# Performance work log

Measured on AMD Instinct MI355X. Metric: run time of the kernel, lower is better.

## Reference

```python
import jax, jax.numpy as jnp
import numpy as np

SEQ, BATCH, IN_DIM, HID, OUT = 512, 256, 300, 256, 2


def setup_inputs() -> dict:
    key = jax.random.key(0)
    ks = jax.random.split(key, 7)
    s_ih = 1.0 / np.sqrt(HID)
    return {
        "x": jax.random.normal(ks[0], (SEQ, BATCH, IN_DIM), jnp.float32),
        "W_ih": jax.random.uniform(ks[1], (HID, IN_DIM), jnp.float32, -s_ih, s_ih),
        "W_hh": jax.random.uniform(ks[2], (HID, HID), jnp.float32, -s_ih, s_ih),
        "b_ih": jax.random.uniform(ks[3], (HID,), jnp.float32, -s_ih, s_ih),
        "b_hh": jax.random.uniform(ks[4], (HID,), jnp.float32, -s_ih, s_ih),
        "W_fc": jax.random.uniform(ks[5], (OUT, HID), jnp.float32, -s_ih, s_ih),
        "b_fc": jax.random.uniform(ks[6], (OUT,), jnp.float32, -s_ih, s_ih),
    }


def reference(x, W_ih, W_hh, b_ih, b_hh, W_fc, b_fc):
    # Precompute input projection for all timesteps at once: [T, B, H]
    xp = jnp.einsum('tbi,hi->tbh', x, W_ih) + b_ih + b_hh

    def step(h, xt):
        h_new = jnp.tanh(xt + h @ W_hh.T)
        return h_new, None

    h0 = jnp.zeros((x.shape[1], W_hh.shape[0]), x.dtype)
    hT, _ = jax.lax.scan(step, h0, xp)  # hT: [B, H]
    # Dropout(0.3) is identity in eval mode.
    logits = hT @ W_fc.T + b_fc  # [B, 2]
    return jax.nn.log_softmax(logits, axis=-1)
```

## Files before the change

kernel.cpp:

```cpp
#include <hip/hip_runtime.h>
#include <hip/hip_bf16.h>
#include <cstdint>
#include <cstddef>

#define SEQ 512
#define BATCH 256
#define IN_DIM 300
#define HID 256

typedef __attribute__((ext_vector_type(8))) short bf16x8;
typedef __attribute__((ext_vector_type(4))) float f32x4;
typedef __attribute__((ext_vector_type(4))) unsigned int u32x4;

__device__ __forceinline__ unsigned short f2bf(float f) {
  union { float f; unsigned int u; } v; v.f = f;
  unsigned int u = v.u;
  return (unsigned short)((u + 0x7fffu + ((u >> 16) & 1u)) >> 16);
}
__device__ __forceinline__ unsigned short f2bf_fast(float f) {
  union { float f; unsigned int u; } v; v.f = f;
  return (unsigned short)((v.u + 0x8000u) >> 16);
}
__device__ __forceinline__ float bitsf(unsigned int u) {
  union { unsigned int u; float f; } v; v.u = u; return v.f;
}
__device__ __forceinline__ unsigned int cvtpk(float lo, float hi) {
  union { __hip_bfloat162 h; unsigned int u; } c;
  c.h = __float22bfloat162_rn(make_float2(lo, hi));
  return c.u;
}
__device__ __forceinline__ bf16x8 cvt8(float a0,float a1,float a2,float a3,
                                       float a4,float a5,float a6,float a7) {
  union { __hip_bfloat162 h2[4]; bf16x8 v; } c;
  c.h2[0] = __float22bfloat162_rn(make_float2(a0, a1));
  c.h2[1] = __float22bfloat162_rn(make_float2(a2, a3));
  c.h2[2] = __float22bfloat162_rn(make_float2(a4, a5));
  c.h2[3] = __float22bfloat162_rn(make_float2(a6, a7));
  return c.v;
}
__device__ __forceinline__ void barrier_lgkm() {
  asm volatile("s_waitcnt lgkmcnt(0)" ::: "memory");
  __builtin_amdgcn_s_barrier();
  asm volatile("" ::: "memory");
}

__global__ __launch_bounds__(256) void conv_wih(const float* __restrict__ w,
                                                unsigned short* __restrict__ w_bf) {
  int idx = blockIdx.x * 256 + threadIdx.x;
  int n = idx / 320, k = idx - n * 320;
  float v = (k < IN_DIM) ? w[n * IN_DIM + k] : 0.f;
  w_bf[idx] = f2bf(v);
}

__global__ __launch_bounds__(512) void gemm_xp(const float* __restrict__ x,
    const unsigned short* __restrict__ w_bf, const float* __restrict__ b_ih,
    const float* __restrict__ b_hh, unsigned int* __restrict__ xp2)
{
  __shared__ unsigned int a_lds[128][20];
  const int tid  = threadIdx.x;
  const int wave = tid >> 6;
  const int lane = tid & 63;
  const int l15  = lane & 15;
  const int quad = lane >> 4;
  const long m0  = (long)blockIdx.x * 128;

  bf16x8 wf[2][10];
  #pragma unroll
  for (int nt = 0; nt < 2; ++nt) {
    const unsigned short* wp = w_bf + (size_t)(wave*32 + nt*16 + l15) * 320 + quad*8;
    #pragma unroll
    for (int kc = 0; kc < 10; ++kc)
      wf[nt][kc] = *(const bf16x8*)(wp + kc*32);
  }

  f32x4 acc[8][2];
  #pragma unroll
  for (int mt = 0; mt < 8; ++mt) {
    acc[mt][0] = (f32x4){0.f, 0.f, 0.f, 0.f};
    acc[mt][1] = (f32x4){0.f, 0.f, 0.f, 0.f};
  }

  const int ar = tid >> 2;
  const int ac = (tid & 3) * 8;
  const float* xrow = x + (size_t)(m0 + ar) * IN_DIM;

  float av[8];
  {
    float2 p0 = *(const float2*)(xrow + ac + 0);
    float2 p1 = *(const float2*)(xrow + ac + 2);
    float2 p2 = *(const float2*)(xrow + ac + 4);
    float2 p3 = *(const float2*)(xrow + ac + 6);
    av[0]=p0.x; av[1]=p0.y; av[2]=p1.x; av[3]=p1.y;
    av[4]=p2.x; av[5]=p2.y; av[6]=p3.x; av[7]=p3.y;
  }

  #pragma unroll
  for (int kc = 0; kc < 10; ++kc) {
    u32x4 pk;
    pk.x = cvtpk(av[0], av[1]);
    pk.y = cvtpk(av[2], av[3]);
    pk.z = cvtpk(av[4], av[5]);
    pk.w = cvtpk(av[6], av[7]);
    *(u32x4*)&a_lds[ar][(tid & 3) * 4] = pk;
    barrier_lgkm();
    if (kc < 9) {
      const int k0 = (kc + 1) * 32;
      const float* src = xrow + k0 + ac;
      if (k0 + ac + 8 <= IN_DIM) {
        float2 p0 = *(const float2*)(src + 0);
        float2 p1 = *(const float2*)(src + 2);
        float2 p2 = *(const float2*)(src + 4);
        float2 p3 = *(const float2*)(src + 6);
        av[0]=p0.x; av[1]=p0.y; av[2]=p1.x; av[3]=p1.y;
        av[4]=p2.x; av[5]=p2.y; av[6]=p3.x; av[7]=p3.y;
      } else {
        #pragma unroll
        for (int j = 0; j < 8; ++j) av[j] = (k0 + ac + j < IN_DIM) ? src[j] : 0.f;
      }
    }
    #pragma unroll
    for (int mt = 0; mt < 8; ++mt) {
      bf16x8 afr = *(const bf16x8*)&a_lds[mt*16 + l15][quad*4];
      acc[mt][0] = __builtin_amdgcn_mfma_f32_16x16x32_bf16(afr, wf[0][kc], acc[mt][0], 0, 0, 0);
      acc[mt][1] = __builtin_amdgcn_mfma_f32_16x16x32_bf16(afr, wf[1][kc], acc[mt][1], 0, 0, 0);
    }
    barrier_lgkm();
  }

  const int t  = (int)(blockIdx.x >> 1);
  const int b4 = ((int)blockIdx.x & 1) * 32;
  #pragma unroll
  for (int nt = 0; nt < 2; ++nt) {
    const int n = wave*32 + nt*16 + l15;
    const float kb = 2.0f * (b_ih[n] + b_hh[n]);
    const int tid_lo = wave*64 + nt*16 + l15;
    #pragma unroll
    for (int mt = 0; mt < 8; ++mt) {
      const int g = b4 + mt*4 + quad;
      const size_t base = ((size_t)t*64 + g) * 512;
      float y0 = fmaf(2.0f, acc[mt][nt][0], kb);
      float y1 = fmaf(2.0f, acc[mt][nt][1], kb);
      float y2 = fmaf(2.0f, acc[mt][nt][2], kb);
      float y3 = fmaf(2.0f, acc[mt][nt][3], kb);
      xp2[base + tid_lo]      = cvtpk(y0, y1);
      xp2[base + tid_lo + 32] = cvtpk(y2, y3);
    }
  }
}

__global__ __launch_bounds__(512) void rnn_scan(const float* __restrict__ W_hh,
    const unsigned int* __restrict__ xp2, float* __restrict__ hT)
{
  __shared__ alignas(16) unsigned short hbuf[2][4 * 272];
  const int tid  = threadIdx.x;
  const int wave = tid >> 6;
  const int lane = tid & 63;
  const int l15  = lane & 15;
  const int quad = lane >> 4;
  const int g = blockIdx.x;
  const int c0 = wave * 32;

  bf16x8 wf[2][8];
  #pragma unroll
  for (int nt = 0; nt < 2; ++nt) {
    const int n = c0 + nt*16 + l15;
    #pragma unroll
    for (int kc = 0; kc < 8; ++kc) {
      const float* src = W_hh + n*HID + kc*32 + quad*8;
      float4 p0 = *(const float4*)src;
      float4 p1 = *(const float4*)(src + 4);
      wf[nt][kc] = cvt8(p0.x,p0.y,p0.z,p0.w,p1.x,p1.y,p1.z,p1.w);
    }
  }

  const int rb    = (quad >> 1) * 2;
  const int col_e = c0 + (quad & 1) * 16 + l15;
  const int abase = (l15 & 3) * 272 + quad * 8;

  for (int i = tid; i < 4 * 272; i += 512) hbuf[0][i] = 0;

  const unsigned int* xbase = xp2 + (size_t)g * 512 + tid;

  __syncthreads();

  unsigned int xq[16], xqn[16];
  #pragma unroll
  for (int j = 0; j < 16; ++j)
    xq[j] = xbase[(size_t)j * 32768];

  for (int tc = 0; tc < SEQ / 16; ++tc) {
    if (tc < SEQ/16 - 1) {
      const unsigned int* pn = xbase + (size_t)(tc + 1) * 16 * 32768;
      #pragma unroll
      for (int j = 0; j < 16; ++j)
        xqn[j] = pn[(size_t)j * 32768];
    }
    #pragma unroll
    for (int j = 0; j < 16; ++j) {
      const int cur = j & 1;
      bf16x8 afr[8];
      #pragma unroll
      for (int kc = 0; kc < 8; ++kc)
        afr[kc] = *(const bf16x8*)&hbuf[cur][abase + kc*32];
      f32x4 a0A = (f32x4){0.f,0.f,0.f,0.f}, a0B = a0A, a1A = a0A, a1B = a0A;
      #pragma unroll
      for (int kc = 0; kc < 8; kc += 2) {
        a0A = __builtin_amdgcn_mfma_f32_16x16x32_bf16(afr[kc],   wf[0][kc],   a0A, 0, 0, 0);
        a1A = __builtin_amdgcn_mfma_f32_16x16x32_bf16(afr[kc],   wf[1][kc],   a1A, 0, 0, 0);
        a0B = __builtin_amdgcn_mfma_f32_16x16x32_bf16(afr[kc+1], wf[0][kc+1], a0B, 0, 0, 0);
        a1B = __builtin_amdgcn_mfma_f32_16x16x32_bf16(afr[kc+1], wf[1][kc+1], a1B, 0, 0, 0);
      }
      f32x4 acc0 = a0A + a0B;
      f32x4 acc1 = a1A + a1B;
      f32x4 a = (quad & 1) ? acc1 : acc0;
      float s0 = (quad >> 1) ? a[2] : a[0];
      float s1 = (quad >> 1) ? a[3] : a[1];
      float xv0 = bitsf(xq[j] << 16);
      float xv1 = bitsf(xq[j] & 0xffff0000u);
      float y0 = fmaf(2.0f, s0, xv0);
      float y1 = fmaf(2.0f, s1, xv1);
      float h0 = fmaf(-2.0f, __builtin_amdgcn_rcpf(__expf(y0) + 1.0f), 1.0f);
      float h1 = fmaf(-2.0f, __builtin_amdgcn_rcpf(__expf(y1) + 1.0f), 1.0f);
      if (j < 15 || tc < SEQ/16 - 1) {
        hbuf[1 - cur][ rb      * 272 + col_e] = f2bf_fast(h0);
        hbuf[1 - cur][(rb + 1) * 272 + col_e] = f2bf_fast(h1);
      } else {
        hT[(size_t)(g*4 + rb    ) * HID + col_e] = h0;
        hT[(size_t)(g*4 + rb + 1) * HID + col_e] = h1;
      }
      barrier_lgkm();
    }
    if (tc < SEQ/16 - 1) {
      #pragma unroll
      for (int j = 0; j < 16; ++j)
        xq[j] = xqn[j];
    }
  }
}

__global__ __launch_bounds__(64) void fc_head(const float* __restrict__ hT,
    const float* __restrict__ W_fc, const float* __restrict__ b_fc,
    float* __restrict__ out)
{
  const int b = blockIdx.x;
  const int l = threadIdx.x;
  float s0 = 0.f, s1 = 0.f;
  #pragma unroll
  for (int j0 = 0; j0 < HID; j0 += 64) {
    float h = hT[(size_t)b * HID + j0 + l];
    s0 += h * W_fc[j0 + l];
    s1 += h * W_fc[HID + j0 + l];
  }
  #pragma unroll
  for (int off = 32; off > 0; off >>= 1) {
    s0 += __shfl_xor(s0, off, 64);
    s1 += __shfl_xor(s1, off, 64);
  }
  if (l == 0) {
    float l0 = s0 + b_fc[0], l1 = s1 + b_fc[1];
    float m = fmaxf(l0, l1);
    float lse = m + logf(expf(l0 - m) + expf(l1 - m));
    out[b*2 + 0] = l0 - lse;
    out[b*2 + 1] = l1 - lse;
  }
}

extern "C" void kernel_launch(void* const* d_in, const int* in_sizes, int n_in,
                              void* d_out, int out_size, void* d_ws, size_t ws_size,
                              hipStream_t stream) {
  const float* x    = (const float*)d_in[0];
  const float* W_ih = (const float*)d_in[1];
  const float* W_hh = (const float*)d_in[2];
  const float* b_ih = (const float*)d_in[3];
  const float* b_hh = (const float*)d_in[4];
  const float* W_fc = (const float*)d_in[5];
  const float* b_fc = (const float*)d_in[6];
  float* out = (float*)d_out;

  const size_t xp_bytes = (size_t)SEQ * BATCH * HID * 2;
  const size_t wb_bytes = (size_t)256 * 320 * 2;
  const size_t ht_bytes = (size_t)BATCH * HID * 4;
  if (ws_size < xp_bytes + wb_bytes + ht_bytes) return;

  char* ws = (char*)d_ws;
  unsigned int*   xp2  = (unsigned int*)ws;
  unsigned short* w_bf = (unsigned short*)(ws + xp_bytes);
  float*          hT   = (float*)(ws + xp_bytes + wb_bytes);

  hipLaunchKernelGGL(conv_wih, dim3(320),  dim3(256), 0, stream, W_ih, w_bf);
  hipLaunchKernelGGL(gemm_xp,  dim3(1024), dim3(512), 0, stream, x, w_bf, b_ih, b_hh, xp2);
  hipLaunchKernelGGL(rnn_scan, dim3(64),   dim3(512), 0, stream, W_hh, xp2, hT);
  hipLaunchKernelGGL(fc_head,  dim3(BATCH), dim3(64), 0, stream, hT, W_fc, b_fc, out);
}
```

Baseline: 492.5 us.

## Fuse input projection and FC head into the recurrent scan kernel

Each recurrent block now computes its own input projection on the fly, one window of 8 timesteps at a time. It stages x in LDS as bf16 and runs a small MFMA GEMM between windows, which removes the large xp intermediate written to and read from global memory and the separate gemm_xp launch. The next window's x rows are prefetched into registers during the scan steps. The FC head and log-softmax also move into the same kernel via LDS, which drops the hT round trip and a launch. In exchange, the input GEMM now runs on only 64 blocks and sits on the serial critical path between windows, so it can lengthen the scan.

```diff
diff --git a/kernel.cpp b/kernel.cpp
--- a/kernel.cpp
+++ b/kernel.cpp
@@ -10,7 +10,6 @@
 
 typedef __attribute__((ext_vector_type(8))) short bf16x8;
 typedef __attribute__((ext_vector_type(4))) float f32x4;
-typedef __attribute__((ext_vector_type(4))) unsigned int u32x4;
 
 __device__ __forceinline__ unsigned short f2bf(float f) {
   union { float f; unsigned int u; } v; v.f = f;
@@ -47,120 +46,86 @@
 __global__ __launch_bounds__(256) void conv_wih(const float* __restrict__ w,
                                                 unsigned short* __restrict__ w_bf) {
   int idx = blockIdx.x * 256 + threadIdx.x;
-  int n = idx / 320, k = idx - n * 320;
+  int j    = idx & 7;
+  int l15  = (idx >> 3) & 15;
+  int quad = (idx >> 7) & 3;
+  int t    = idx >> 9;
+  int n16  = t / 10;
+  int kc   = t - n16 * 10;
+  int n = n16 * 16 + l15;
+  int k = kc * 32 + quad * 8 + j;
   float v = (k < IN_DIM) ? w[n * IN_DIM + k] : 0.f;
   w_bf[idx] = f2bf(v);
 }
 
-__global__ __launch_bounds__(512) void gemm_xp(const float* __restrict__ x,
+__device__ __forceinline__ void win_gemm(const unsigned int* __restrict__ a_lds,
+    unsigned int* __restrict__ xpbuf, const bf16x8 wfi[2][10],
+    float kb0, float kb1, int wave, int l15, int quad)
+{
+  f32x4 acc[2][2];
+  #pragma unroll
+  for (int mt = 0; mt < 2; ++mt) {
+    acc[mt][0] = (f32x4){0.f,0.f,0.f,0.f};
+    acc[mt][1] = (f32x4){0.f,0.f,0.f,0.f};
+  }
+  #pragma unroll
+  for (int kc = 0; kc < 10; ++kc) {
+    bf16x8 afr0 = *(const bf16x8*)&a_lds[(     l15) * 164 + kc*16 + quad*4];
+    bf16x8 afr1 = *(const bf16x8*)&a_lds[(16 + l15) * 164 + kc*16 + quad*4];
+    acc[0][0] = __builtin_amdgcn_mfma_f32_16x16x32_bf16(afr0, wfi[0][kc], acc[0][0], 0, 0, 0);
+    acc[0][1] = __builtin_amdgcn_mfma_f32_16x16x32_bf16(afr0, wfi[1][kc], acc[0][1], 0, 0, 0);
+    acc[1][0] = __builtin_amdgcn_mfma_f32_16x16x32_bf16(afr1, wfi[0][kc], acc[1][0], 0, 0, 0);
+    acc[1][1] = __builtin_amdgcn_mfma_f32_16x16x32_bf16(afr1, wfi[1][kc], acc[1][1], 0, 0, 0);
+  }
+  #pragma unroll
+  for (int nt = 0; nt < 2; ++nt) {
+    const float kb = nt ? kb1 : kb0;
+    const int tid_s = wave*64 + nt*16 + l15;
+    #pragma unroll
+    for (int mt = 0; mt < 2; ++mt) {
+      const int idx = (mt*4 + quad) * 512 + tid_s;
+      float y0 = fmaf(2.0f, acc[mt][nt][0], kb);
+      float y1 = fmaf(2.0f, acc[mt][nt][1], kb);
+      float y2 = fmaf(2.0f, acc[mt][nt][2], kb);
+      float y3 = fmaf(2.0f, acc[mt][nt][3], kb);
+      xpbuf[idx]      = cvtpk(y0, y1);
+      xpbuf[idx + 32] = cvtpk(y2, y3);
+    }
+  }
+}
+
+__device__ __forceinline__ void win_stage(unsigned int* __restrict__ a_lds,
+    const float4* __restrict__ xr, const int* __restrict__ sidx, int tid)
+{
+  #pragma unroll
+  for (int i = 0; i < 5; ++i)
+    if (i < 4 || tid < 352) {
+      uint2 pk2;
+      pk2.x = cvtpk(xr[i].x, xr[i].y);
+      pk2.y = cvtpk(xr[i].z, xr[i].w);
+      *(uint2*)&a_lds[sidx[i]] = pk2;
+    }
+}
+
+__global__ __launch_bounds__(512, 2) void rnn_all(const float* __restrict__ x,
     const unsigned short* __restrict__ w_bf, const float* __restrict__ b_ih,
-    const float* __restrict__ b_hh, unsigned int* __restrict__ xp2)
+    const float* __restrict__ b_hh, const float* __restrict__ W_hh,
+    const float* __restrict__ W_fc, const float* __restrict__ b_fc,
+    float* __restrict__ out)
 {
-  __shared__ unsigned int a_lds[128][20];
+  __shared__ alignas(16) unsigned int   xpbuf[8 * 512];
+  __shared__ alignas(16) unsigned int   a_lds[32 * 164];
+  __shared__ alignas(16) unsigned short hbuf[2][1088];
+
   const int tid  = threadIdx.x;
   const int wave = tid >> 6;
   const int lane = tid & 63;
   const int l15  = lane & 15;
   const int quad = lane >> 4;
-  const long m0  = (long)blockIdx.x * 128;
-
-  bf16x8 wf[2][10];
-  #pragma unroll
-  for (int nt = 0; nt < 2; ++nt) {
-    const unsigned short* wp = w_bf + (size_t)(wave*32 + nt*16 + l15) * 320 + quad*8;
-    #pragma unroll
-    for (int kc = 0; kc < 10; ++kc)
-      wf[nt][kc] = *(const bf16x8*)(wp + kc*32);
-  }
-
-  f32x4 acc[8][2];
-  #pragma unroll
-  for (int mt = 0; mt < 8; ++mt) {
-    acc[mt][0] = (f32x4){0.f, 0.f, 0.f, 0.f};
-    acc[mt][1] = (f32x4){0.f, 0.f, 0.f, 0.f};
-  }
-
-  const int ar = tid >> 2;
-  const int ac = (tid & 3) * 8;
-  const float* xrow = x + (size_t)(m0 + ar) * IN_DIM;
-
-  float av[8];
-  {
-    float2 p0 = *(const float2*)(xrow + ac + 0);
-    float2 p1 = *(const float2*)(xrow + ac + 2);
-    float2 p2 = *(const float2*)(xrow + ac + 4);
-    float2 p3 = *(const float2*)(xrow + ac + 6);
-    av[0]=p0.x; av[1]=p0.y; av[2]=p1.x; av[3]=p1.y;
-    av[4]=p2.x; av[5]=p2.y; av[6]=p3.x; av[7]=p3.y;
-  }
-
-  #pragma unroll
-  for (int kc = 0; kc < 10; ++kc) {
-    u32x4 pk;
-    pk.x = cvtpk(av[0], av[1]);
-    pk.y = cvtpk(av[2], av[3]);
-    pk.z = cvtpk(av[4], av[5]);
-    pk.w = cvtpk(av[6], av[7]);
-    *(u32x4*)&a_lds[ar][(tid & 3) * 4] = pk;
-    barrier_lgkm();
-    if (kc < 9) {
-      const int k0 = (kc + 1) * 32;
-      const float* src = xrow + k0 + ac;
-      if (k0 + ac + 8 <= IN_DIM) {
-        float2 p0 = *(const float2*)(src + 0);
-        float2 p1 = *(const float2*)(src + 2);
-        float2 p2 = *(const float2*)(src + 4);
-        float2 p3 = *(const float2*)(src + 6);
-        av[0]=p0.x; av[1]=p0.y; av[2]=p1.x; av[3]=p1.y;
-        av[4]=p2.x; av[5]=p2.y; av[6]=p3.x; av[7]=p3.y;
-      } else {
-        #pragma unroll
-        for (int j = 0; j < 8; ++j) av[j] = (k0 + ac + j < IN_DIM) ? src[j] : 0.f;
-      }
-    }
-    #pragma unroll
-    for (int mt = 0; mt < 8; ++mt) {
-      bf16x8 afr = *(const bf16x8*)&a_lds[mt*16 + l15][quad*4];
-      acc[mt][0] = __builtin_amdgcn_mfma_f32_16x16x32_bf16(afr, wf[0][kc], acc[mt][0], 0, 0, 0);
-      acc[mt][1] = __builtin_amdgcn_mfma_f32_16x16x32_bf16(afr, wf[1][kc], acc[mt][1], 0, 0, 0);
-    }
-    barrier_lgkm();
-  }
-
-  const int t  = (int)(blockIdx.x >> 1);
-  const int b4 = ((int)blockIdx.x & 1) * 32;
-  #pragma unroll
-  for (int nt = 0; nt < 2; ++nt) {
-    const int n = wave*32 + nt*16 + l15;
-    const float kb = 2.0f * (b_ih[n] + b_hh[n]);
-    const int tid_lo = wave*64 + nt*16 + l15;
-    #pragma unroll
-    for (int mt = 0; mt < 8; ++mt) {
-      const int g = b4 + mt*4 + quad;
-      const size_t base = ((size_t)t*64 + g) * 512;
-      float y0 = fmaf(2.0f, acc[mt][nt][0], kb);
-      float y1 = fmaf(2.0f, acc[mt][nt][1], kb);
-      float y2 = fmaf(2.0f, acc[mt][nt][2], kb);
-      float y3 = fmaf(2.0f, acc[mt][nt][3], kb);
-      xp2[base + tid_lo]      = cvtpk(y0, y1);
-      xp2[base + tid_lo + 32] = cvtpk(y2, y3);
-    }
-  }
-}
-
-__global__ __launch_bounds__(512) void rnn_scan(const float* __restrict__ W_hh,
-    const unsigned int* __restrict__ xp2, float* __restrict__ hT)
-{
-  __shared__ alignas(16) unsigned short hbuf[2][4 * 272];
-  const int tid  = threadIdx.x;
-  const int wave = tid >> 6;
-  const int lane = tid & 63;
-  const int l15  = lane & 15;
-  const int quad = lane >> 4;
-  const int g = blockIdx.x;
-  const int c0 = wave * 32;
-
-  bf16x8 wf[2][8];
+  const int g    = blockIdx.x;
+  const int c0   = wave * 32;
+
+  bf16x8 wfh[2][8];
   #pragma unroll
   for (int nt = 0; nt < 2; ++nt) {
     const int n = c0 + nt*16 + l15;
@@ -169,35 +134,64 @@
       const float* src = W_hh + n*HID + kc*32 + quad*8;
       float4 p0 = *(const float4*)src;
       float4 p1 = *(const float4*)(src + 4);
-      wf[nt][kc] = cvt8(p0.x,p0.y,p0.z,p0.w,p1.x,p1.y,p1.z,p1.w);
-    }
+      wfh[nt][kc] = cvt8(p0.x,p0.y,p0.z,p0.w,p1.x,p1.y,p1.z,p1.w);
+    }
+  }
+  bf16x8 wfi[2][10];
+  #pragma unroll
+  for (int nt = 0; nt < 2; ++nt) {
+    const unsigned short* wp =
+        w_bf + ((size_t)((wave*2 + nt)*10)*4 + quad)*128 + (size_t)l15*8;
+    #pragma unroll
+    for (int kc = 0; kc < 10; ++kc)
+      wfi[nt][kc] = *(const bf16x8*)(wp + (size_t)kc*512);
+  }
+  const float kb0 = 2.0f * (b_ih[c0 + l15]      + b_hh[c0 + l15]);
+  const float kb1 = 2.0f * (b_ih[c0 + 16 + l15] + b_hh[c0 + 16 + l15]);
+
+  unsigned int voff[5]; int sidx[5];
+  #pragma unroll
+  for (int i = 0; i < 5; ++i) {
+    const int e = tid + i * 512;
+    const int row = e / 75;
+    const int c4  = e - row * 75;
+    const int t_loc = row >> 2, b_loc = row & 3;
+    voff[i] = (unsigned)(((t_loc * 256 + 4 * g + b_loc) * 300 + c4 * 4) * 4);
+    sidx[i] = row * 164 + c4 * 2;
   }
 
   const int rb    = (quad >> 1) * 2;
   const int col_e = c0 + (quad & 1) * 16 + l15;
   const int abase = (l15 & 3) * 272 + quad * 8;
 
-  for (int i = tid; i < 4 * 272; i += 512) hbuf[0][i] = 0;
-
-  const unsigned int* xbase = xp2 + (size_t)g * 512 + tid;
-
+  for (int i = tid; i < 1088; i += 512) hbuf[0][i] = 0;
+  if (tid < 320) a_lds[(tid / 10) * 164 + 150 + (tid % 10)] = 0;
+
+  float4 xr[5];
+  #pragma unroll
+  for (int i = 0; i < 5; ++i)
+    if (i < 4 || tid < 352)
+      xr[i] = *(const float4*)((const char*)x + voff[i]);
   __syncthreads();
-
-  unsigned int xq[16], xqn[16];
-  #pragma unroll
-  for (int j = 0; j < 16; ++j)
-    xq[j] = xbase[(size_t)j * 32768];
-
-  for (int tc = 0; tc < SEQ / 16; ++tc) {
-    if (tc < SEQ/16 - 1) {
-      const unsigned int* pn = xbase + (size_t)(tc + 1) * 16 * 32768;
-      #pragma unroll
-      for (int j = 0; j < 16; ++j)
-        xqn[j] = pn[(size_t)j * 32768];
-    }
-    #pragma unroll
-    for (int j = 0; j < 16; ++j) {
+  win_stage(a_lds, xr, sidx, tid);
+  barrier_lgkm();
+  win_gemm(a_lds, xpbuf, wfi, kb0, kb1, wave, l15, quad);
+  barrier_lgkm();
+
+  const size_t WSTRIDE = (size_t)8 * 256 * 300 * 4;
+
+  for (int w = 0; w < 64; ++w) {
+    const char* pn = (const char*)x + (size_t)(w + 1) * WSTRIDE;
+    #pragma unroll
+    for (int j = 0; j < 8; ++j) {
+      if (j == 0 && w < 63) {
+        #pragma unroll
+        for (int i = 0; i < 5; ++i)
+          if (i < 4 || tid < 352)
+            xr[i] = *(const float4*)(pn + voff[i]);
+      }
       const int cur = j & 1;
+      const unsigned int xqj = xpbuf[j * 512 + tid];
       bf16x8 afr[8];
       #pragma unroll
       for (int kc = 0; kc < 8; ++kc)
@@ -205,63 +199,62 @@
       f32x4 a0A = (f32x4){0.f,0.f,0.f,0.f}, a0B = a0A, a1A = a0A, a1B = a0A;
       #pragma unroll
       for (int kc = 0; kc < 8; kc += 2) {
-        a0A = __builtin_amdgcn_mfma_f32_16x16x32_bf16(afr[kc],   wf[0][kc],   a0A, 0, 0, 0);
-        a1A = __builtin_amdgcn_mfma_f32_16x16x32_bf16(afr[kc],   wf[1][kc],   a1A, 0, 0, 0);
-        a0B = __builtin_amdgcn_mfma_f32_16x16x32_bf16(afr[kc+1], wf[0][kc+1], a0B, 0, 0, 0);
-        a1B = __builtin_amdgcn_mfma_f32_16x16x32_bf16(afr[kc+1], wf[1][kc+1], a1B, 0, 0, 0);
+        a0A = __builtin_amdgcn_mfma_f32_16x16x32_bf16(afr[kc],   wfh[0][kc],   a0A, 0, 0, 0);
+        a1A = __builtin_amdgcn_mfma_f32_16x16x32_bf16(afr[kc],   wfh[1][kc],   a1A, 0, 0, 0);
+        a0B = __builtin_amdgcn_mfma_f32_16x16x32_bf16(afr[kc+1], wfh[0][kc+1], a0B, 0, 0, 0);
+        a1B = __builtin_amdgcn_mfma_f32_16x16x32_bf16(afr[kc+1], wfh[1][kc+1], a1B, 0, 0, 0);
       }
+      if (j == 5 && w < 63)
+        win_stage(a_lds, xr, sidx, tid);
       f32x4 acc0 = a0A + a0B;
       f32x4 acc1 = a1A + a1B;
       f32x4 a = (quad & 1) ? acc1 : acc0;
       float s0 = (quad >> 1) ? a[2] : a[0];
       float s1 = (quad >> 1) ? a[3] : a[1];
-      float xv0 = bitsf(xq[j] << 16);
-      float xv1 = bitsf(xq[j] & 0xffff0000u);
+      float xv0 = bitsf(xqj << 16);
+      float xv1 = bitsf(xqj & 0xffff0000u);
       float y0 = fmaf(2.0f, s0, xv0);
       float y1 = fmaf(2.0f, s1, xv1);
       float h0 = fmaf(-2.0f, __builtin_amdgcn_rcpf(__expf(y0) + 1.0f), 1.0f);
       float h1 = fmaf(-2.0f, __builtin_amdgcn_rcpf(__expf(y1) + 1.0f), 1.0f);
-      if (j < 15 || tc < SEQ/16 - 1) {
+      if (w == 63 && j == 7) {
+        float* fcb = (float*)xpbuf;
+        fcb[ rb      * 256 + col_e] = h0;
+        fcb[(rb + 1) * 256 + col_e] = h1;
+      } else {
         hbuf[1 - cur][ rb      * 272 + col_e] = f2bf_fast(h0);
         hbuf[1 - cur][(rb + 1) * 272 + col_e] = f2bf_fast(h1);
-      } else {
-        hT[(size_t)(g*4 + rb    ) * HID + col_e] = h0;
-        hT[(size_t)(g*4 + rb + 1) * HID + col_e] = h1;
       }
       barrier_lgkm();
     }
-    if (tc < SEQ/16 - 1) {
-      #pragma unroll
-      for (int j = 0; j < 16; ++j)
-        xq[j] = xqn[j];
-    }
-  }
-}
-
-__global__ __launch_bounds__(64) void fc_head(const float* __restrict__ hT,
-    const float* __restrict__ W_fc, const float* __restrict__ b_fc,
-    float* __restrict__ out)
-{
-  const int b = blockIdx.x;
-  const int l = threadIdx.x;
-  float s0 = 0.f, s1 = 0.f;
-  #pragma unroll
-  for (int j0 = 0; j0 < HID; j0 += 64) {
-    float h = hT[(size_t)b * HID + j0 + l];
-    s0 += h * W_fc[j0 + l];
-    s1 += h * W_fc[HID + j0 + l];
-  }
-  #pragma unroll
-  for (int off = 32; off > 0; off >>= 1) {
-    s0 += __shfl_xor(s0, off, 64);
-    s1 += __shfl_xor(s1, off, 64);
-  }
-  if (l == 0) {
-    float l0 = s0 + b_fc[0], l1 = s1 + b_fc[1];
-    float m = fmaxf(l0, l1);
-    float lse = m + logf(expf(l0 - m) + expf(l1 - m));
-    out[b*2 + 0] = l0 - lse;
-    out[b*2 + 1] = l1 - lse;
+    if (w < 63) {
+      win_gemm(a_lds, xpbuf, wfi, kb0, kb1, wave, l15, quad);
+      barrier_lgkm();
+    }
+  }
+
+  if (wave < 4) {
+    const float* fcb = (const float*)xpbuf + wave * 256;
+    float s0 = 0.f, s1 = 0.f;
+    #pragma unroll
+    for (int j0 = 0; j0 < HID; j0 += 64) {
+      float h = fcb[j0 + lane];
+      s0 += h * W_fc[j0 + lane];
+      s1 += h * W_fc[HID + j0 + lane];
+    }
+    #pragma unroll
+    for (int off = 32; off > 0; off >>= 1) {
+      s0 += __shfl_xor(s0, off, 64);
+      s1 += __shfl_xor(s1, off, 64);
+    }
+    if (lane == 0) {
+      const int b = g * 4 + wave;
+      float l0 = s0 + b_fc[0], l1 = s1 + b_fc[1];
+      float m = fmaxf(l0, l1);
+      float lse = m + logf(expf(l0 - m) + expf(l1 - m));
+      out[b*2 + 0] = l0 - lse;
+      out[b*2 + 1] = l1 - lse;
+    }
   }
 }
 
@@ -277,18 +270,11 @@
   const float* b_fc = (const float*)d_in[6];
   float* out = (float*)d_out;
 
-  const size_t xp_bytes = (size_t)SEQ * BATCH * HID * 2;
   const size_t wb_bytes = (size_t)256 * 320 * 2;
-  const size_t ht_bytes = (size_t)BATCH * HID * 4;
-  if (ws_size < xp_bytes + wb_bytes + ht_bytes) return;
-
-  char* ws = (char*)d_ws;
-  unsigned int*   xp2  = (unsigned int*)ws;
-  unsigned short* w_bf = (unsigned short*)(ws + xp_bytes);
-  float*          hT   = (float*)(ws + xp_bytes + wb_bytes);
-
-  hipLaunchKernelGGL(conv_wih, dim3(320),  dim3(256), 0, stream, W_ih, w_bf);
-  hipLaunchKernelGGL(gemm_xp,  dim3(1024), dim3(512), 0, stream, x, w_bf, b_ih, b_hh, xp2);
-  hipLaunchKernelGGL(rnn_scan, dim3(64),   dim3(512), 0, stream, W_hh, xp2, hT);
-  hipLaunchKernelGGL(fc_head,  dim3(BATCH), dim3(64), 0, stream, hT, W_fc, b_fc, out);
-}
+  if (ws_size < wb_bytes) return;
+  unsigned short* w_bf = (unsigned short*)d_ws;
+
+  hipLaunchKernelGGL(conv_wih, dim3(320), dim3(256), 0, stream, W_ih, w_bf);
+  hipLaunchKernelGGL(rnn_all,  dim3(64),  dim3(512), 0, stream,
+                     x, w_bf, b_ih, b_hh, W_hh, W_fc, b_fc, out);
+}
```

Measured after the change: 530.1 us. 7.6% more time.
